# Optimization experiments

Hardware: AMD Instinct MI355X
Metric: run time of the kernel (lower is better)

## Reference

```python
import jax, jax.numpy as jnp
import numpy as np

N = 63001
F_IN = 512
F_OUT = 256
E = 2_000_000
LRELU_ALPHA = 0.2


def setup_inputs() -> dict:
    key = jax.random.key(0)
    ks = jax.random.split(key, 10)
    x = jax.random.normal(ks[0], (N, F_IN), dtype=jnp.float32)
    values = jax.random.uniform(ks[1], (E,), dtype=jnp.float32)
    edge_index = jax.random.randint(ks[2], (2, E), 0, N, dtype=jnp.int32)
    # learned params: conv1d kernel_size=1 == dense matmuls
    W = jax.random.normal(ks[3], (F_IN, F_OUT), dtype=jnp.float32) * (1.0 / np.sqrt(F_IN))
    a1 = jax.random.normal(ks[4], (F_OUT,), dtype=jnp.float32) * (1.0 / np.sqrt(F_OUT))
    b1 = jnp.zeros((), dtype=jnp.float32)
    a2 = jax.random.normal(ks[5], (F_OUT,), dtype=jnp.float32) * (1.0 / np.sqrt(F_OUT))
    b2 = jnp.zeros((), dtype=jnp.float32)
    b_out = jnp.zeros((F_OUT,), dtype=jnp.float32)
    return {"x": x, "values": values, "edge_index": edge_index,
            "W": W, "a1": a1, "b1": b1, "a2": a2, "b2": b2, "b_out": b_out}


def reference(x, values, edge_index, W, a1, b1, a2, b2, b_out):
    src = edge_index[0]  # row index i of sparse adjacency entry
    dst = edge_index[1]  # col index j

    # conv1d(kernel=1) projections == matmuls
    seq_fts = x @ W                      # [N, F_out]
    f1 = seq_fts @ a1 + b1               # [N]
    f2 = seq_fts @ a2 + b2               # [N]

    # edgewise logits: s_ij * f1_i + s_ij * f2_j  (sparse_add of two masked broadcasts)
    logits = values * (f1[src] + f2[dst])           # [E]
    logits = jax.nn.leaky_relu(logits, LRELU_ALPHA)

    # sparse row-wise softmax over edges grouped by src
    m = jax.ops.segment_max(logits, src, num_segments=N)   # [N]
    p = jnp.exp(logits - m[src])                            # [E]
    denom = jax.ops.segment_sum(p, src, num_segments=N)     # [N]
    coefs = p / denom[src]                                  # [E]

    # SPMM: out_i = sum_j coef_ij * seq_fts_j
    out = jnp.zeros((N, F_OUT), dtype=seq_fts.dtype)
    out = out.at[src].add(coefs[:, None] * seq_fts[dst])

    out = out + b_out                                       # bias_add
    return jax.nn.elu(out)
```

## Files before the change

### kernel.cpp

```cpp
#include <hip/hip_runtime.h>
#include <hip/hip_bf16.h>
#include <cstdint>
#include <cstddef>

#define FIN 512
#define FOUT 256
#define LRELU 0.2f
#define NBKT 8
#define BSH 13

typedef __attribute__((ext_vector_type(8))) short bf16x8;
typedef __attribute__((ext_vector_type(8))) unsigned short u16x8;
typedef __attribute__((ext_vector_type(4))) float f32x4;
typedef _Float16 h16x2 __attribute__((ext_vector_type(2)));

#define PERM_LO 0x05040100u
#define PERM_HI 0x07060302u
#define ONE2H   0x3C003C00u

__device__ inline ushort f2bf(float f) {
    __hip_bfloat16 h = __float2bfloat16(f);
    union { __hip_bfloat16 h; ushort u; } c; c.h = h;
    return c.u;
}
__device__ inline ushort f2h(float f) {
    union { _Float16 h; ushort u; } c; c.h = (_Float16)f;
    return c.u;
}
__device__ inline h16x2 u2h2(uint32_t u) {
    union { uint32_t u; h16x2 h; } c; c.u = u;
    return c.h;
}
__device__ inline float hdot2(h16x2 pp, uint32_t sv, float acc) {
    return __builtin_amdgcn_fdot2(pp, u2h2(sv), acc, false);
}

__global__ void prep_wt(const float* __restrict__ W, ushort* __restrict__ WT)
{
    const int idx = blockIdx.x * blockDim.x + threadIdx.x;
    if (idx < FIN * FOUT) {
        const int k = idx >> 8, n = idx & 255;
        WT[(size_t)n * FIN + k] = f2bf(W[(size_t)k * FOUT + n]);
    }
}

#define BM 128
#define BK 64
__global__ __launch_bounds__(512) void gemm_bf16(
    const float* __restrict__ A,
    const ushort* __restrict__ BT,
    ushort* __restrict__ Ch,
    const float* __restrict__ a1, const float* __restrict__ a2,
    const float* __restrict__ b1, const float* __restrict__ b2,
    float* __restrict__ f1, float* __restrict__ f2,
    int M)
{
    __shared__ ushort As[BM * BK];
    __shared__ ushort Bs[FOUT * BK];
    __shared__ float f1s[BM][2];
    __shared__ float f2s[BM][2];
    const int t = threadIdx.x;
    const int lane = t & 63, w = t >> 6;
    const int wm = w & 3, wn = w >> 2;
    const int brow = blockIdx.x * BM;

    f32x4 acc[2][8] = {};

    const int ar = t >> 2;
    const int ak = (t & 3) << 4;

    const int bcol8 = (lane >> 3);
    const int bslot = lane & 7;
    const int bcdat = bslot ^ (bcol8 & 7);

    for (int k0 = 0; k0 < FIN; k0 += BK) {
#pragma unroll
        for (int j = 0; j < 4; ++j) {
            const int grp = w * 4 + j;
            const int col = grp * 8 + bcol8;
            const ushort* gsrc = BT + (size_t)col * FIN + k0 + bcdat * 8;
            ushort* ldst = &Bs[grp * 512];
            __builtin_amdgcn_global_load_lds(
                (const __attribute__((address_space(1))) void*)gsrc,
                (__attribute__((address_space(3))) void*)ldst, 16, 0, 0);
        }
        {
            f32x4 v0, v1, v2, v3;
            const int grow = brow + ar;
            if (grow < M) {
                const f32x4* p = (const f32x4*)(A + (size_t)grow * FIN + k0 + ak);
                v0 = __builtin_nontemporal_load(p + 0);
                v1 = __builtin_nontemporal_load(p + 1);
                v2 = __builtin_nontemporal_load(p + 2);
                v3 = __builtin_nontemporal_load(p + 3);
            } else {
                v0 = v1 = v2 = v3 = (f32x4)0.f;
            }
            u16x8 w0, w1;
            w0[0]=f2bf(v0[0]); w0[1]=f2bf(v0[1]); w0[2]=f2bf(v0[2]); w0[3]=f2bf(v0[3]);
            w0[4]=f2bf(v1[0]); w0[5]=f2bf(v1[1]); w0[6]=f2bf(v1[2]); w0[7]=f2bf(v1[3]);
            w1[0]=f2bf(v2[0]); w1[1]=f2bf(v2[1]); w1[2]=f2bf(v2[2]); w1[3]=f2bf(v2[3]);
            w1[4]=f2bf(v3[0]); w1[5]=f2bf(v3[1]); w1[6]=f2bf(v3[2]); w1[7]=f2bf(v3[3]);
            const int c0 = ((ak >> 3) + 0) ^ (ar & 7);
            const int c1 = ((ak >> 3) + 1) ^ (ar & 7);
            *(u16x8*)(&As[ar * BK + (c0 << 3)]) = w0;
            *(u16x8*)(&As[ar * BK + (c1 << 3)]) = w1;
        }
        __syncthreads();

#pragma unroll
        for (int kk = 0; kk < 2; ++kk) {
            const int kc = kk * 4 + (lane >> 4);
            bf16x8 af[2], bfr[8];
#pragma unroll
            for (int m = 0; m < 2; ++m) {
                const int row = wm * 32 + m * 16 + (lane & 15);
                af[m] = *(const bf16x8*)(&As[row * BK + ((kc ^ (row & 7)) << 3)]);
            }
#pragma unroll
            for (int n = 0; n < 8; ++n) {
                const int col = wn * 128 + n * 16 + (lane & 15);
                bfr[n] = *(const bf16x8*)(&Bs[col * BK + ((kc ^ (col & 7)) << 3)]);
            }
#pragma unroll
            for (int m = 0; m < 2; ++m)
#pragma unroll
                for (int n = 0; n < 8; ++n)
                    acc[m][n] = __builtin_amdgcn_mfma_f32_16x16x32_bf16(
                        af[m], bfr[n], acc[m][n], 0, 0, 0);
        }
        __syncthreads();
    }

    float a1c[8], a2c[8];
#pragma unroll
    for (int n = 0; n < 8; ++n) {
        const int col = wn * 128 + n * 16 + (lane & 15);
        a1c[n] = a1[col];
        a2c[n] = a2[col];
    }
    const int cbase = wn * 128 + (lane & 15);
#pragma unroll
    for (int m = 0; m < 2; ++m) {
#pragma unroll
        for (int reg = 0; reg < 4; ++reg) {
            const int rloc = wm * 32 + m * 16 + (lane >> 4) * 4 + reg;
            const int r = brow + rloc;
            float p1 = 0.f, p2 = 0.f;
#pragma unroll
            for (int n = 0; n < 8; ++n) {
                p1 += acc[m][n][reg] * a1c[n];
                p2 += acc[m][n][reg] * a2c[n];
            }
#pragma unroll
            for (int off = 1; off < 16; off <<= 1) {
                p1 += __shfl_xor(p1, off);
                p2 += __shfl_xor(p2, off);
            }
            if ((lane & 15) == 0) {
                f1s[rloc][wn] = p1;
                f2s[rloc][wn] = p2;
            }
            if (r < M) {
#pragma unroll
                for (int n = 0; n < 8; ++n)
                    Ch[(size_t)r * FOUT + cbase + n * 16] = f2h(acc[m][n][reg]);
            }
        }
    }
    __syncthreads();
    if (t < BM) {
        const int r = brow + t;
        if (r < M) {
            f1[r] = f1s[t][0] + f1s[t][1] + b1[0];
            f2[r] = f2s[t][0] + f2s[t][1] + b2[0];
        }
    }
}

__global__ void cnt_kernel(const int* __restrict__ src, const int* __restrict__ dst,
                           int* __restrict__ cnt, int E)
{
    int i = (blockIdx.x * blockDim.x + threadIdx.x) * 4;
    if (i + 4 <= E) {
        const int4 s = *(const int4*)(src + i);
        const int4 d = *(const int4*)(dst + i);
        atomicAdd(&cnt[s.x * NBKT + (d.x >> BSH)], 1);
        atomicAdd(&cnt[s.y * NBKT + (d.y >> BSH)], 1);
        atomicAdd(&cnt[s.z * NBKT + (d.z >> BSH)], 1);
        atomicAdd(&cnt[s.w * NBKT + (d.w >> BSH)], 1);
    } else {
        for (; i < E; ++i) atomicAdd(&cnt[src[i] * NBKT + (dst[i] >> BSH)], 1);
    }
}

__global__ __launch_bounds__(1024) void scan_blk(const int* __restrict__ cnt,
                                                 int* __restrict__ btot, int K)
{
    __shared__ int s[1024];
    const int t = threadIdx.x;
    const int idx = blockIdx.x * 1024 + t;
    s[t] = (idx < K) ? cnt[idx] : 0;
    __syncthreads();
    for (int off = 512; off; off >>= 1) {
        if (t < off) s[t] += s[t + off];
        __syncthreads();
    }
    if (t == 0) btot[blockIdx.x] = s[0];
}

__global__ __launch_bounds__(1024) void scan_top(const int* __restrict__ btot,
                                                 int* __restrict__ boff, int nb)
{
    __shared__ int s[1024];
    const int t = threadIdx.x;
    const int mine = (t < nb) ? btot[t] : 0;
    s[t] = mine;
    __syncthreads();
    for (int off = 1; off < 1024; off <<= 1) {
        const int u = (t >= off) ? s[t - off] : 0;
        __syncthreads();
        s[t] += u;
        __syncthreads();
    }
    if (t < nb) boff[t] = s[t] - mine;
}

__global__ __launch_bounds__(1024) void scan_out(const int* __restrict__ cnt,
                                                 const int* __restrict__ boff,
                                                 int* __restrict__ koff,
                                                 int* __restrict__ cursor, int K)
{
    __shared__ int s[1024];
    const int t = threadIdx.x;
    const int b = blockIdx.x;
    const int idx = b * 1024 + t;
    const int v = (idx < K) ? cnt[idx] : 0;
    s[t] = v;
    __syncthreads();
    for (int off = 1; off < 1024; off <<= 1) {
        const int u = (t >= off) ? s[t - off] : 0;
        __syncthreads();
        s[t] += u;
        __syncthreads();
    }
    if (idx < K) {
        const int e = boff[b] + s[t] - v;
        koff[idx] = e;
        cursor[idx] = e;
    }
    if (idx == K - 1) koff[K] = boff[b] + s[t];
}

__global__ void scatter_p(const int* __restrict__ src, const int* __restrict__ dst,
                          const float* __restrict__ values,
                          const float* __restrict__ f1, const float* __restrict__ f2,
                          int* __restrict__ cursor,
                          uint32_t* __restrict__ pd, int E)
{
    const int i = blockIdx.x * blockDim.x + threadIdx.x;
    if (i < E) {
        const int s = src[i];
        const int d = dst[i];
        float lg = values[i] * (f1[s] + f2[d]);
        lg = (lg > 0.f) ? lg : LRELU * lg;
        const float p = __expf(lg);
        const int slot = atomicAdd(&cursor[s * NBKT + (d >> BSH)], 1);
        pd[slot] = ((uint32_t)d << 16) | (uint32_t)f2h(p);
    }
}

__global__ __launch_bounds__(256) void spmm_kernel(
    const ushort* __restrict__ seq,
    const uint32_t* __restrict__ pd,
    const int* __restrict__ koff, const float* __restrict__ b_out,
    float* __restrict__ out, int N)
{
    const int w = threadIdx.x >> 6, lane = threadIdx.x & 63;
    const int row = blockIdx.x * 4 + w;
    if (row >= N) return;
    const int start = __builtin_amdgcn_readfirstlane(koff[row * NBKT]);
    const int end   = __builtin_amdgcn_readfirstlane(koff[(row + 1) * NBKT]);

    const ushort* seql = seq + lane * 4;
    float acc0 = 0.f, acc1 = 0.f, acc2 = 0.f, acc3 = 0.f, den = 0.f;
    const h16x2 one2 = u2h2(ONE2H);

    int t = start;
    for (; t + 8 <= end; t += 8) {
        uint32_t q[8];
#pragma unroll
        for (int j = 0; j < 8; ++j) q[j] = pd[t + j];
        uint2 s[8];
#pragma unroll
        for (int j = 0; j < 8; ++j)
            s[j] = *(const uint2*)(seql + (size_t)(q[j] >> 16) * FOUT);
#pragma unroll
        for (int j = 0; j < 8; j += 2) {
            const h16x2 pp = u2h2((q[j] & 0xffffu) | (q[j + 1] << 16));
            acc0 = hdot2(pp, __builtin_amdgcn_perm(s[j+1].x, s[j].x, PERM_LO), acc0);
            acc1 = hdot2(pp, __builtin_amdgcn_perm(s[j+1].x, s[j].x, PERM_HI), acc1);
            acc2 = hdot2(pp, __builtin_amdgcn_perm(s[j+1].y, s[j].y, PERM_LO), acc2);
            acc3 = hdot2(pp, __builtin_amdgcn_perm(s[j+1].y, s[j].y, PERM_HI), acc3);
            den  = hdot2(pp, ONE2H, den);
        }
    }
    for (; t + 2 <= end; t += 2) {
        const uint32_t q0 = pd[t], q1 = pd[t + 1];
        const uint2 s0 = *(const uint2*)(seql + (size_t)(q0 >> 16) * FOUT);
        const uint2 s1 = *(const uint2*)(seql + (size_t)(q1 >> 16) * FOUT);
        const h16x2 pp = u2h2((q0 & 0xffffu) | (q1 << 16));
        acc0 = hdot2(pp, __builtin_amdgcn_perm(s1.x, s0.x, PERM_LO), acc0);
        acc1 = hdot2(pp, __builtin_amdgcn_perm(s1.x, s0.x, PERM_HI), acc1);
        acc2 = hdot2(pp, __builtin_amdgcn_perm(s1.y, s0.y, PERM_LO), acc2);
        acc3 = hdot2(pp, __builtin_amdgcn_perm(s1.y, s0.y, PERM_HI), acc3);
        den  = hdot2(pp, ONE2H, den);
    }
    if (t < end) {
        const uint32_t q0 = pd[t];
        const uint2 s0 = *(const uint2*)(seql + (size_t)(q0 >> 16) * FOUT);
        const h16x2 pp = u2h2(q0 & 0xffffu);
        acc0 = hdot2(pp, __builtin_amdgcn_perm(s0.x, s0.x, PERM_LO), acc0);
        acc1 = hdot2(pp, __builtin_amdgcn_perm(s0.x, s0.x, PERM_HI), acc1);
        acc2 = hdot2(pp, __builtin_amdgcn_perm(s0.y, s0.y, PERM_LO), acc2);
        acc3 = hdot2(pp, __builtin_amdgcn_perm(s0.y, s0.y, PERM_HI), acc3);
        den  = hdot2(pp, ONE2H, den);
    }

    const float inv = (end > start) ? 1.f / den : 0.f;
    const float4 bo = *(const float4*)(b_out + lane * 4);
    f32x4 o;
    o[0] = acc0 * inv + bo.x;
    o[1] = acc1 * inv + bo.y;
    o[2] = acc2 * inv + bo.z;
    o[3] = acc3 * inv + bo.w;
    o[0] = (o[0] > 0.f) ? o[0] : expm1f(o[0]);
    o[1] = (o[1] > 0.f) ? o[1] : expm1f(o[1]);
    o[2] = (o[2] > 0.f) ? o[2] : expm1f(o[2]);
    o[3] = (o[3] > 0.f) ? o[3] : expm1f(o[3]);
    __builtin_nontemporal_store(o, (f32x4*)(out + (size_t)row * FOUT + lane * 4));
}

extern "C" void kernel_launch(void* const* d_in, const int* in_sizes, int n_in,
                              void* d_out, int out_size, void* d_ws, size_t ws_size,
                              hipStream_t stream)
{
    const float* x      = (const float*)d_in[0];
    const float* values = (const float*)d_in[1];
    const int*   ei     = (const int*)d_in[2];
    const float* W      = (const float*)d_in[3];
    const float* a1     = (const float*)d_in[4];
    const float* b1     = (const float*)d_in[5];
    const float* a2     = (const float*)d_in[6];
    const float* b2     = (const float*)d_in[7];
    const float* b_out  = (const float*)d_in[8];
    float* out = (float*)d_out;

    const int N = in_sizes[0] / FIN;
    const int E = in_sizes[1];
    const int* src = ei;
    const int* dst = ei + E;
    const int K = N * NBKT;

    auto alignup = [](size_t v) { return (v + 255) & ~(size_t)255; };
    char* ws = (char*)d_ws;
    size_t off = 0;
    ushort*   seqh   = (ushort*)(ws + off);   off = alignup(off + (size_t)N * FOUT * 2);
    ushort*   WT     = (ushort*)(ws + off);   off = alignup(off + (size_t)FIN * FOUT * 2);
    float*    f1     = (float*)(ws + off);    off = alignup(off + (size_t)N * 4);
    float*    f2     = (float*)(ws + off);    off = alignup(off + (size_t)N * 4);
    int*      cnt    = (int*)(ws + off);      off = alignup(off + (size_t)K * 4);
    int*      koff   = (int*)(ws + off);      off = alignup(off + (size_t)(K + 1) * 4);
    int*      cursor = (int*)(ws + off);      off = alignup(off + (size_t)K * 4);
    int*      btot   = (int*)(ws + off);      off = alignup(off + (size_t)1024 * 4);
    int*      boff   = (int*)(ws + off);      off = alignup(off + (size_t)1024 * 4);
    uint32_t* pd     = (uint32_t*)(ws + off); off = alignup(off + (size_t)E * 4);
    (void)ws_size;

    const int nbk = (K + 1023) / 1024;

    hipMemsetAsync(cnt, 0, (size_t)K * 4, stream);

    cnt_kernel<<<(E / 4 + 255) / 256, 256, 0, stream>>>(src, dst, cnt, E);
    scan_blk<<<nbk, 1024, 0, stream>>>(cnt, btot, K);
    scan_top<<<1, 1024, 0, stream>>>(btot, boff, nbk);
    scan_out<<<nbk, 1024, 0, stream>>>(cnt, boff, koff, cursor, K);

    prep_wt<<<(FIN * FOUT + 255) / 256, 256, 0, stream>>>(W, WT);
    gemm_bf16<<<(N + BM - 1) / BM, 512, 0, stream>>>(x, WT, seqh, a1, a2, b1, b2,
                                                     f1, f2, N);

    scatter_p<<<(E + 255) / 256, 256, 0, stream>>>(src, dst, values, f1, f2,
                                                   cursor, pd, E);

    spmm_kernel<<<(N + 3) / 4, 256, 0, stream>>>(seqh, pd, koff, b_out, out, N);
}
```

Before: 389.0 us.

## Record per-edge bucket positions during counting to drop scatter-phase atomics

The counting kernel now stores the value returned by each atomic increment as a 16-bit per-edge position. The scatter kernel then computes its slot as koff plus that position instead of doing a second atomicAdd on a cursor array, and writes with nontemporal stores. The cursor array goes away, and the destination bucketing is made finer (16 buckets of 4096 columns instead of 8) for better gather locality in the SpMM. The cost is an extra 4 MB array written and read, a larger count/scan array, and the assumption that no bucket holds more than 65535 edges.

```diff
diff --git a/kernel.cpp b/kernel.cpp
--- a/kernel.cpp
+++ b/kernel.cpp
@@ -6,8 +6,8 @@
 #define FIN 512
 #define FOUT 256
 #define LRELU 0.2f
-#define NBKT 8
-#define BSH 13
+#define NBKT 16
+#define BSH 12
 
 typedef __attribute__((ext_vector_type(8))) short bf16x8;
 typedef __attribute__((ext_vector_type(8))) unsigned short u16x8;
@@ -47,8 +47,7 @@
 #define BM 128
 #define BK 64
 __global__ __launch_bounds__(512) void gemm_bf16(
-    const float* __restrict__ A,
-    const ushort* __restrict__ BT,
+    const float* __restrict__ A, const ushort* __restrict__ BT,
     ushort* __restrict__ Ch,
     const float* __restrict__ a1, const float* __restrict__ a2,
     const float* __restrict__ b1, const float* __restrict__ b2,
@@ -178,19 +177,22 @@
     }
 }
 
-__global__ void cnt_kernel(const int* __restrict__ src, const int* __restrict__ dst,
-                           int* __restrict__ cnt, int E)
+__global__ void pos_kernel(const int* __restrict__ src, const int* __restrict__ dst,
+                           int* __restrict__ cnt, ushort* __restrict__ pos, int E)
 {
     int i = (blockIdx.x * blockDim.x + threadIdx.x) * 4;
     if (i + 4 <= E) {
         const int4 s = *(const int4*)(src + i);
         const int4 d = *(const int4*)(dst + i);
-        atomicAdd(&cnt[s.x * NBKT + (d.x >> BSH)], 1);
-        atomicAdd(&cnt[s.y * NBKT + (d.y >> BSH)], 1);
-        atomicAdd(&cnt[s.z * NBKT + (d.z >> BSH)], 1);
-        atomicAdd(&cnt[s.w * NBKT + (d.w >> BSH)], 1);
+        ushort4 p;
+        p.x = (ushort)atomicAdd(&cnt[s.x * NBKT + (d.x >> BSH)], 1);
+        p.y = (ushort)atomicAdd(&cnt[s.y * NBKT + (d.y >> BSH)], 1);
+        p.z = (ushort)atomicAdd(&cnt[s.z * NBKT + (d.z >> BSH)], 1);
+        p.w = (ushort)atomicAdd(&cnt[s.w * NBKT + (d.w >> BSH)], 1);
+        *(ushort4*)(pos + i) = p;
     } else {
-        for (; i < E; ++i) atomicAdd(&cnt[src[i] * NBKT + (dst[i] >> BSH)], 1);
+        for (; i < E; ++i)
+            pos[i] = (ushort)atomicAdd(&cnt[src[i] * NBKT + (dst[i] >> BSH)], 1);
     }
 }
 
@@ -228,8 +230,7 @@
 
 __global__ __launch_bounds__(1024) void scan_out(const int* __restrict__ cnt,
                                                  const int* __restrict__ boff,
-                                                 int* __restrict__ koff,
-                                                 int* __restrict__ cursor, int K)
+                                                 int* __restrict__ koff, int K)
 {
     __shared__ int s[1024];
     const int t = threadIdx.x;
@@ -244,18 +245,14 @@
         s[t] += u;
         __syncthreads();
     }
-    if (idx < K) {
-        const int e = boff[b] + s[t] - v;
-        koff[idx] = e;
-        cursor[idx] = e;
-    }
-    if (idx == K - 1) koff[K] = boff[b] + s[t];
+    if (idx < K)      koff[idx] = boff[b] + s[t] - v;
+    if (idx == K - 1) koff[K]   = boff[b] + s[t];
 }
 
 __global__ void scatter_p(const int* __restrict__ src, const int* __restrict__ dst,
-                          const float* __restrict__ values,
+                          const float* __restrict__ values, const ushort* __restrict__ pos,
                           const float* __restrict__ f1, const float* __restrict__ f2,
-                          int* __restrict__ cursor,
+                          const int* __restrict__ koff,
                           uint32_t* __restrict__ pd, int E)
 {
     const int i = blockIdx.x * blockDim.x + threadIdx.x;
@@ -265,8 +262,8 @@
         float lg = values[i] * (f1[s] + f2[d]);
         lg = (lg > 0.f) ? lg : LRELU * lg;
         const float p = __expf(lg);
-        const int slot = atomicAdd(&cursor[s * NBKT + (d >> BSH)], 1);
-        pd[slot] = ((uint32_t)d << 16) | (uint32_t)f2h(p);
+        const int slot = koff[s * NBKT + (d >> BSH)] + (int)pos[i];
+        __builtin_nontemporal_store(((uint32_t)d << 16) | (uint32_t)f2h(p), &pd[slot]);
     }
 }
 
@@ -284,7 +281,6 @@
 
     const ushort* seql = seq + lane * 4;
     float acc0 = 0.f, acc1 = 0.f, acc2 = 0.f, acc3 = 0.f, den = 0.f;
-    const h16x2 one2 = u2h2(ONE2H);
 
     int t = start;
     for (; t + 8 <= end; t += 8) {
@@ -365,33 +361,33 @@
     auto alignup = [](size_t v) { return (v + 255) & ~(size_t)255; };
     char* ws = (char*)d_ws;
     size_t off = 0;
-    ushort*   seqh   = (ushort*)(ws + off);   off = alignup(off + (size_t)N * FOUT * 2);
-    ushort*   WT     = (ushort*)(ws + off);   off = alignup(off + (size_t)FIN * FOUT * 2);
-    float*    f1     = (float*)(ws + off);    off = alignup(off + (size_t)N * 4);
-    float*    f2     = (float*)(ws + off);    off = alignup(off + (size_t)N * 4);
-    int*      cnt    = (int*)(ws + off);      off = alignup(off + (size_t)K * 4);
-    int*      koff   = (int*)(ws + off);      off = alignup(off + (size_t)(K + 1) * 4);
-    int*      cursor = (int*)(ws + off);      off = alignup(off + (size_t)K * 4);
-    int*      btot   = (int*)(ws + off);      off = alignup(off + (size_t)1024 * 4);
-    int*      boff   = (int*)(ws + off);      off = alignup(off + (size_t)1024 * 4);
-    uint32_t* pd     = (uint32_t*)(ws + off); off = alignup(off + (size_t)E * 4);
+    ushort*   seqh = (ushort*)(ws + off);   off = alignup(off + (size_t)N * FOUT * 2);
+    ushort*   WT   = (ushort*)(ws + off);   off = alignup(off + (size_t)FIN * FOUT * 2);
+    float*    f1   = (float*)(ws + off);    off = alignup(off + (size_t)N * 4);
+    float*    f2   = (float*)(ws + off);    off = alignup(off + (size_t)N * 4);
+    int*      cnt  = (int*)(ws + off);      off = alignup(off + (size_t)K * 4);
+    int*      koff = (int*)(ws + off);      off = alignup(off + (size_t)(K + 1) * 4);
+    int*      btot = (int*)(ws + off);      off = alignup(off + (size_t)1024 * 4);
+    int*      boff = (int*)(ws + off);      off = alignup(off + (size_t)1024 * 4);
+    ushort*   pos  = (ushort*)(ws + off);   off = alignup(off + (size_t)E * 2);
+    uint32_t* pd   = (uint32_t*)(ws + off); off = alignup(off + (size_t)E * 4);
     (void)ws_size;
 
     const int nbk = (K + 1023) / 1024;
 
     hipMemsetAsync(cnt, 0, (size_t)K * 4, stream);
 
-    cnt_kernel<<<(E / 4 + 255) / 256, 256, 0, stream>>>(src, dst, cnt, E);
+    pos_kernel<<<(E / 4 + 255) / 256, 256, 0, stream>>>(src, dst, cnt, pos, E);
     scan_blk<<<nbk, 1024, 0, stream>>>(cnt, btot, K);
     scan_top<<<1, 1024, 0, stream>>>(btot, boff, nbk);
-    scan_out<<<nbk, 1024, 0, stream>>>(cnt, boff, koff, cursor, K);
+    scan_out<<<nbk, 1024, 0, stream>>>(cnt, boff, koff, K);
 
     prep_wt<<<(FIN * FOUT + 255) / 256, 256, 0, stream>>>(W, WT);
     gemm_bf16<<<(N + BM - 1) / BM, 512, 0, stream>>>(x, WT, seqh, a1, a2, b1, b2,
                                                      f1, f2, N);
 
-    scatter_p<<<(E + 255) / 256, 256, 0, stream>>>(src, dst, values, f1, f2,
-                                                   cursor, pd, E);
+    scatter_p<<<(E + 255) / 256, 256, 0, stream>>>(src, dst, values, pos, f1, f2,
+                                                   koff, pd, E);
 
     spmm_kernel<<<(N + 3) / 4, 256, 0, stream>>>(seqh, pd, koff, b_out, out, N);
 }
```

Result: faster. 350.8 us (-9.8%).
